# Kernel tuning notes

Hardware: AMD Instinct MI355X
Metric: run time of the kernel (lower is better)

## Reference

```python
import jax, jax.numpy as jnp
import numpy as np

BS, D, NC, N, C, K = 8192, 1024, 64, 100000, 1000, 50


def setup_inputs() -> dict:
    key = jax.random.key(0)
    k1, k2, k3, k4, k5 = jax.random.split(key, 5)
    return {
        "train_embedding": jax.random.normal(k1, (BS, D), dtype=jnp.float32),
        # concept initialized uniform in [-0.5, 0.5] as in init_concept
        "concept": jax.random.uniform(k2, (D, NC), dtype=jnp.float32, minval=-0.5, maxval=0.5),
        "bank": jax.random.normal(k3, (N, D), dtype=jnp.float32),
        "W_h": jax.random.normal(k4, (D, C), dtype=jnp.float32) * 0.02,
        "b_h": jax.random.normal(k5, (C,), dtype=jnp.float32) * 0.02,
        "topk": K,
    }


def reference(train_embedding, concept, bank, W_h, b_h, topk):
    # h_x: linear classifier head
    def h_x(z):
        return z @ W_h + b_h

    # projection onto concept subspace: C (C^T C)^{-1} C^T
    G = concept.T @ concept                      # [nc, nc]
    proj_matrix = concept @ jnp.linalg.inv(G) @ concept.T  # [D, D]
    proj = train_embedding @ proj_matrix.T       # (proj_matrix @ X^T)^T -> [bs, D]
    y_pred = h_x(proj)                           # [bs, C]
    orig_pred = h_x(train_embedding)             # [bs, C]

    # batched per-concept Euclidean distance to the whole bank: [nc, N]
    bank_sq = jnp.sum(bank * bank, axis=1)       # [N]
    con_sq = jnp.sum(concept * concept, axis=0)  # [nc]
    d2 = con_sq[:, None] - 2.0 * (concept.T @ bank.T) + bank_sq[None, :]
    dist = jnp.sqrt(jnp.maximum(d2, 0.0))
    # topk SMALLEST distances per concept
    _, idx = jax.lax.top_k(-dist, topk)          # idx: [nc, k]
    knn = bank[idx]                              # [nc, k, D] gather

    # L_sparse_1: mean over concepts of (c . mean_k knn)
    dots = jnp.einsum('dn,nkd->n', concept, knn) / topk  # [nc]
    L_sparse_1 = jnp.mean(dots)

    nc = concept.shape[1]
    eye = jnp.eye(nc, dtype=concept.dtype)
    L_sparse_2 = jnp.mean(G * (1.0 - eye))       # off-diagonal mean
    norm_metrics = jnp.mean(G * eye)             # diagonal mean

    return (orig_pred, y_pred, L_sparse_1, L_sparse_2, norm_metrics)
```

## Files before the change

### kernel.cpp

```cpp
#include <hip/hip_runtime.h>
#include <cstddef>

#define BSZ   8192
#define DIM   1024
#define NCON  64
#define NBANK 100000
#define NCLS  1000
#define TOPK  50
#define NCHUNK 32
#define CHUNK  3125
#define CHUNKP 3328

#define Y_OFF 8192000
#define S_OFF 16384000

typedef __attribute__((ext_vector_type(8))) short bf16x8;
typedef __attribute__((ext_vector_type(4))) float f32x4;

__device__ __forceinline__ short f2bf(float x) {
    unsigned u = __builtin_bit_cast(unsigned, x);
    unsigned r = (u + 0x7fffu + ((u >> 16) & 1u)) >> 16;
    return (short)r;
}

__device__ __forceinline__ bf16x8 pack8(f32x4 a, f32x4 b) {
    bf16x8 p;
    p[0] = f2bf(a[0]); p[1] = f2bf(a[1]); p[2] = f2bf(a[2]); p[3] = f2bf(a[3]);
    p[4] = f2bf(b[0]); p[5] = f2bf(b[1]); p[6] = f2bf(b[2]); p[7] = f2bf(b[3]);
    return p;
}

__device__ __forceinline__ void gload16(const void* g, void* l) {
    __builtin_amdgcn_global_load_lds(
        (__attribute__((address_space(1))) void*)g,
        (__attribute__((address_space(3))) void*)l,
        16, 0, 0);
}

__global__ void __launch_bounds__(256) prep_kernel(const float* __restrict__ cpt,
                                                   const float* __restrict__ Wh,
                                                   short* __restrict__ WhT,
                                                   short* __restrict__ cptT) {
    __shared__ short Ts[64][65];
    int b = blockIdx.x;
    int t = threadIdx.x;
    if (b < 256) {
        int k0 = (b & 15) * 64, n0 = (b >> 4) * 64;
        #pragma unroll
        for (int i = 0; i < 16; ++i) {
            int u = i * 256 + t;
            int kL = u >> 6, nL = u & 63;
            int n = n0 + nL;
            Ts[kL][nL] = (n < NCLS) ? f2bf(Wh[(size_t)(k0 + kL) * NCLS + n]) : (short)0;
        }
        __syncthreads();
        #pragma unroll
        for (int i = 0; i < 16; ++i) {
            int u = i * 256 + t;
            int nL = u >> 6, kL = u & 63;
            WhT[(size_t)(n0 + nL) * DIM + k0 + kL] = Ts[kL][nL];
        }
    } else {
        int q = b - 256;
        #pragma unroll
        for (int i = 0; i < 16; ++i) {
            int u = q * 4096 + i * 256 + t;
            int d = u >> 6, n = u & 63;
            cptT[n * DIM + d] = f2bf(cpt[u]);
        }
    }
}

__global__ void __launch_bounds__(256) mid_kernel(const float* __restrict__ bank,
                                                  const float* __restrict__ X,
                                                  const short* __restrict__ cptT,
                                                  const short* __restrict__ WhT,
                                                  short* __restrict__ Xbf,
                                                  short* __restrict__ XCbf,
                                                  float* __restrict__ key,
                                                  float* __restrict__ bank_sq,
                                                  short* __restrict__ MbfT,
                                                  float* __restrict__ G,
                                                  short* __restrict__ invGbf) {
    __shared__ __align__(16) char smem[40960];
    int b = blockIdx.x;
    int t = threadIdx.x;
    int wid = t >> 6, l = t & 63, lr = l & 15, lg = l >> 4;
    if (b < 8) {
        int c0 = b * 128;
        f32x4 acc[4][2] = {};
        for (int kk = 0; kk < DIM; kk += 32) {
            bf16x8 af[4], bfr[2];
            #pragma unroll
            for (int mi = 0; mi < 4; ++mi)
                af[mi] = *(const bf16x8*)(cptT + (mi * 16 + lr) * DIM + kk + lg * 8);
            #pragma unroll
            for (int ni = 0; ni < 2; ++ni)
                bfr[ni] = *(const bf16x8*)(WhT + (size_t)(c0 + wid * 32 + ni * 16 + lr) * DIM + kk + lg * 8);
            #pragma unroll
            for (int mi = 0; mi < 4; ++mi)
                #pragma unroll
                for (int ni = 0; ni < 2; ++ni)
                    acc[mi][ni] = __builtin_amdgcn_mfma_f32_16x16x32_bf16(af[mi], bfr[ni], acc[mi][ni], 0, 0, 0);
        }
        #pragma unroll
        for (int mi = 0; mi < 4; ++mi)
            #pragma unroll
            for (int ni = 0; ni < 2; ++ni)
                #pragma unroll
                for (int r = 0; r < 4; ++r) {
                    int m = mi * 16 + lg * 4 + r;
                    int c = c0 + wid * 32 + ni * 16 + lr;
                    MbfT[(size_t)c * NCON + m] = f2bf(acc[mi][ni][r]);
                }
    } else if (b == 8) {
        float* rowk = (float*)smem;
        float* fk = (float*)(smem + 256);
        f32x4 acc[4] = {};
        for (int kk = 0; kk < DIM; kk += 32) {
            bf16x8 af[4], bfr;
            #pragma unroll
            for (int mi = 0; mi < 4; ++mi)
                af[mi] = *(const bf16x8*)(cptT + (mi * 16 + lr) * DIM + kk + lg * 8);
            bfr = *(const bf16x8*)(cptT + (wid * 16 + lr) * DIM + kk + lg * 8);
            #pragma unroll
            for (int mi = 0; mi < 4; ++mi)
                acc[mi] = __builtin_amdgcn_mfma_f32_16x16x32_bf16(af[mi], bfr, acc[mi], 0, 0, 0);
        }
        #pragma unroll
        for (int mi = 0; mi < 4; ++mi)
            #pragma unroll
            for (int r = 0; r < 4; ++r)
                G[(mi * 16 + lg * 4 + r) * 64 + wid * 16 + lr] = acc[mi][r];
        __syncthreads();
        float myA[16];
        #pragma unroll
        for (int s = 0; s < 16; ++s) myA[s] = G[(4 * s + wid) * 64 + l];
        #pragma unroll
        for (int k = 0; k < 64; ++k) {
            if (wid == (k & 3)) rowk[l] = myA[k >> 2];
            if (l == k) {
                #pragma unroll
                for (int s = 0; s < 16; ++s) fk[4 * s + wid] = myA[s];
            }
            __syncthreads();
            float ip = 1.f / rowk[k];
            float rv = rowk[l];
            #pragma unroll
            for (int s = 0; s < 16; ++s) {
                int i = 4 * s + wid;
                float fv = fk[i];
                float nv;
                if (i == k && l == k)      nv = ip;
                else if (i == k)           nv = rv * ip;
                else if (l == k)           nv = -fv * ip;
                else                       nv = myA[s] - fv * (rv * ip);
                myA[s] = nv;
            }
            __syncthreads();
        }
        #pragma unroll
        for (int s = 0; s < 16; ++s) invGbf[(4 * s + wid) * 64 + l] = f2bf(myA[s]);
    } else if (b < 73) {
        int r0 = (b - 9) * 128;
        int r_[2];
        const float* xrow[2];
        #pragma unroll
        for (int ni = 0; ni < 2; ++ni) {
            r_[ni] = r0 + wid * 32 + ni * 16 + lr;
            xrow[ni] = X + (size_t)r_[ni] * DIM + lg * 8;
        }
        f32x4 acc[4][2] = {};
        for (int kk = 0; kk < DIM; kk += 32) {
            bf16x8 af[4];
            #pragma unroll
            for (int mi = 0; mi < 4; ++mi)
                af[mi] = *(const bf16x8*)(cptT + (mi * 16 + lr) * DIM + kk + lg * 8);
            #pragma unroll
            for (int ni = 0; ni < 2; ++ni) {
                f32x4 a = *(const f32x4*)(xrow[ni] + kk);
                f32x4 c = *(const f32x4*)(xrow[ni] + kk + 4);
                bf16x8 pk = pack8(a, c);
                *(bf16x8*)(Xbf + (size_t)r_[ni] * DIM + kk + lg * 8) = pk;
                #pragma unroll
                for (int mi = 0; mi < 4; ++mi)
                    acc[mi][ni] = __builtin_amdgcn_mfma_f32_16x16x32_bf16(af[mi], pk, acc[mi][ni], 0, 0, 0);
            }
        }
        #pragma unroll
        for (int mi = 0; mi < 4; ++mi)
            #pragma unroll
            for (int ni = 0; ni < 2; ++ni)
                #pragma unroll
                for (int r = 0; r < 4; ++r) {
                    int m = mi * 16 + lg * 4 + r;
                    XCbf[(size_t)r_[ni] * NCON + m] = f2bf(acc[mi][ni][r]);
                }
    } else {
        int j0 = (b - 73) * 128;
        int bj[4], bs[4];
        #pragma unroll
        for (int i = 0; i < 4; ++i) {
            int flat = i * 4096 + wid * 1024 + l * 16;
            bj[i] = flat >> 7;
            bs[i] = ((flat >> 4) & 7) ^ (bj[i] & 7);
        }
        int cflat = wid * 1024 + l * 16;
        int cm = cflat >> 6;
        int cs = ((cflat >> 4) & 3) ^ (cm & 3);
        f32x4 acc[4][2] = {};
        float sq[2] = {0.f, 0.f};
        int jrow[2];
        #pragma unroll
        for (int ni = 0; ni < 2; ++ni) jrow[ni] = wid * 32 + ni * 16 + lr;
        #pragma unroll
        for (int i = 0; i < 4; ++i) {
            int jr = j0 + bj[i]; if (jr >= NBANK) jr = NBANK - 1;
            gload16(bank + (size_t)jr * DIM + bs[i] * 4, smem + i * 4096 + wid * 1024);
        }
        gload16(cptT + cm * DIM + cs * 8, smem + 32768 + wid * 1024);
        int buf = 0;
        for (int kk = 0; kk < DIM; kk += 32) {
            __syncthreads();
            int kn = kk + 32;
            int nb = buf ^ 1;
            if (kn < DIM) {
                #pragma unroll
                for (int i = 0; i < 4; ++i) {
                    int jr = j0 + bj[i]; if (jr >= NBANK) jr = NBANK - 1;
                    gload16(bank + (size_t)jr * DIM + kn + bs[i] * 4,
                            smem + nb * 16384 + i * 4096 + wid * 1024);
                }
                gload16(cptT + cm * DIM + kn + cs * 8, smem + 32768 + nb * 4096 + wid * 1024);
            }
            const float* bT = (const float*)(smem + buf * 16384);
            const short* cS = (const short*)(smem + 32768 + buf * 4096);
            bf16x8 af[4];
            #pragma unroll
            for (int mi = 0; mi < 4; ++mi) {
                int m = mi * 16 + lr;
                af[mi] = *(const bf16x8*)(cS + m * 32 + ((lg ^ (m & 3)) << 3));
            }
            #pragma unroll
            for (int ni = 0; ni < 2; ++ni) {
                int j = jrow[ni];
                int g0 = lg * 2, g1 = lg * 2 + 1;
                f32x4 a = *(const f32x4*)(bT + j * 32 + ((g0 ^ (j & 7)) << 2));
                f32x4 c = *(const f32x4*)(bT + j * 32 + ((g1 ^ (j & 7)) << 2));
                sq[ni] += a[0]*a[0] + a[1]*a[1] + a[2]*a[2] + a[3]*a[3]
                        + c[0]*c[0] + c[1]*c[1] + c[2]*c[2] + c[3]*c[3];
                bf16x8 pk = pack8(a, c);
                #pragma unroll
                for (int mi = 0; mi < 4; ++mi)
                    acc[mi][ni] = __builtin_amdgcn_mfma_f32_16x16x32_bf16(af[mi], pk, acc[mi][ni], 0, 0, 0);
            }
            buf ^= 1;
        }
        #pragma unroll
        for (int ni = 0; ni < 2; ++ni) {
            float s = sq[ni];
            s += __shfl_xor(s, 16);
            s += __shfl_xor(s, 32);
            sq[ni] = s;
            int j = j0 + jrow[ni];
            if (j < NBANK && lg == 0) bank_sq[j] = s;
        }
        #pragma unroll
        for (int mi = 0; mi < 4; ++mi)
            #pragma unroll
            for (int ni = 0; ni < 2; ++ni) {
                int j = j0 + jrow[ni];
                if (j < NBANK) {
                    #pragma unroll
                    for (int r = 0; r < 4; ++r) {
                        int m = mi * 16 + lg * 4 + r;
                        key[(size_t)m * NBANK + j] = sq[ni] - 2.f * acc[mi][ni][r];
                    }
                }
            }
    }
}

__global__ void __launch_bounds__(256) topA_kernel(const float* __restrict__ key,
                                                   float* __restrict__ cand_v,
                                                   int* __restrict__ cand_j,
                                                   const short* __restrict__ invGbf,
                                                   const short* __restrict__ MbfT,
                                                   short* __restrict__ M2T) {
    __shared__ float vals[CHUNKP];
    __shared__ float wv[4];
    __shared__ int wj[4];
    int b = blockIdx.x;
    int t = threadIdx.x;
    if (b < 2048) {
        int n = b >> 5;
        int c = b & 31;
        int base = c * CHUNK;
        const float* row = key + (size_t)n * NBANK + base;
        float lv = __builtin_inff();
        int lj = 0x7fffffff;
        #pragma unroll 13
        for (int i = 0; i < 13; ++i) {
            int j = t + i * 256;
            float v = (j < CHUNK) ? row[j] : __builtin_inff();
            vals[j] = v;
            if (v < lv) { lv = v; lj = j; }
        }
        __syncthreads();
        float* cv = cand_v + (size_t)b * TOPK;
        int* cj = cand_j + (size_t)b * TOPK;
        for (int it = 0; it < TOPK; ++it) {
            float bv = lv; int bj = lj;
            #pragma unroll
            for (int o = 32; o > 0; o >>= 1) {
                float ov = __shfl_down(bv, o);
                int oj = __shfl_down(bj, o);
                if (ov < bv || (ov == bv && oj < bj)) { bv = ov; bj = oj; }
            }
            if ((t & 63) == 0) { wv[t >> 6] = bv; wj[t >> 6] = bj; }
            __syncthreads();
            float gv = wv[0]; int gj = wj[0];
            #pragma unroll
            for (int w2 = 1; w2 < 4; ++w2)
                if (wv[w2] < gv || (wv[w2] == gv && wj[w2] < gj)) { gv = wv[w2]; gj = wj[w2]; }
            if (t == 0) { cv[it] = gv; cj[it] = base + gj; }
            if (t == (gj & 255)) {
                vals[gj] = __builtin_inff();
                lv = __builtin_inff(); lj = 0x7fffffff;
                #pragma unroll 13
                for (int i = 0; i < 13; ++i) {
                    int j = t + i * 256;
                    float v = vals[j];
                    if (v < lv) { lv = v; lj = j; }
                }
            }
            __syncthreads();
        }
    } else {
        int c0 = (b - 2048) * 128;
        int wid = t >> 6, l = t & 63, lr = l & 15, lg = l >> 4;
        f32x4 acc[4][2] = {};
        #pragma unroll
        for (int ks = 0; ks < 2; ++ks) {
            bf16x8 af[4], bfr[2];
            #pragma unroll
            for (int mi = 0; mi < 4; ++mi)
                af[mi] = *(const bf16x8*)(invGbf + (mi * 16 + lr) * NCON + ks * 32 + lg * 8);
            #pragma unroll
            for (int ni = 0; ni < 2; ++ni)
                bfr[ni] = *(const bf16x8*)(MbfT + (size_t)(c0 + wid * 32 + ni * 16 + lr) * NCON + ks * 32 + lg * 8);
            #pragma unroll
            for (int mi = 0; mi < 4; ++mi)
                #pragma unroll
                for (int ni = 0; ni < 2; ++ni)
                    acc[mi][ni] = __builtin_amdgcn_mfma_f32_16x16x32_bf16(af[mi], bfr[ni], acc[mi][ni], 0, 0, 0);
        }
        #pragma unroll
        for (int mi = 0; mi < 4; ++mi)
            #pragma unroll
            for (int ni = 0; ni < 2; ++ni)
                #pragma unroll
                for (int r = 0; r < 4; ++r) {
                    int n = mi * 16 + lg * 4 + r;
                    int c = c0 + wid * 32 + ni * 16 + lr;
                    M2T[(size_t)c * NCON + n] = f2bf(acc[mi][ni][r]);
                }
    }
}

__global__ void __launch_bounds__(256) pred_kernel(const short* __restrict__ Xbf,
                                                   const short* __restrict__ WhT,
                                                   const short* __restrict__ XCbf,
                                                   const short* __restrict__ M2T,
                                                   const float* __restrict__ bh,
                                                   const float* __restrict__ cand_v,
                                                   const int* __restrict__ cand_j,
                                                   const float* __restrict__ bank_sq,
                                                   float* __restrict__ orig,
                                                   float* __restrict__ ypred,
                                                   float* __restrict__ dots) {
    __shared__ __align__(16) char smem[32768];
    int b = blockIdx.x;
    int t = threadIdx.x;
    int wid = t >> 6, l = t & 63, lr = l & 15, lg = l >> 4;
    if (b < 512) {
        short* As = (short*)smem;
        short* Bs = (short*)(smem + 16384);
        int c0 = (b & 7) * 128;
        int r0 = (b >> 3) * 128;
        int wr = wid >> 1, wc = wid & 1;
        int srow_off = l >> 3;
        int scol = ((l & 7) ^ (l >> 3)) * 8;
        f32x4 acc[4][4] = {};
        for (int kk = 0; kk < DIM; kk += 64) {
            if (kk) __syncthreads();
            #pragma unroll
            for (int i = 0; i < 4; ++i) {
                int si = wid * 4 + i;
                int row = si * 8 + srow_off;
                gload16(Xbf + (size_t)(r0 + row) * DIM + kk + scol, As + si * 512);
                gload16(WhT + (size_t)(c0 + row) * DIM + kk + scol, Bs + si * 512);
            }
            __syncthreads();
            #pragma unroll
            for (int ks = 0; ks < 2; ++ks) {
                bf16x8 af[4], bfr[4];
                #pragma unroll
                for (int mi = 0; mi < 4; ++mi) {
                    int rr = wr * 64 + mi * 16 + lr;
                    int slot = (ks * 4 + lg) ^ (rr & 7);
                    af[mi] = *(const bf16x8*)(As + rr * 64 + slot * 8);
                }
                #pragma unroll
                for (int ni = 0; ni < 4; ++ni) {
                    int cc = wc * 64 + ni * 16 + lr;
                    int slot = (ks * 4 + lg) ^ (cc & 7);
                    bfr[ni] = *(const bf16x8*)(Bs + cc * 64 + slot * 8);
                }
                #pragma unroll
                for (int mi = 0; mi < 4; ++mi)
                    #pragma unroll
                    for (int ni = 0; ni < 4; ++ni)
                        acc[mi][ni] = __builtin_amdgcn_mfma_f32_16x16x32_bf16(af[mi], bfr[ni], acc[mi][ni], 0, 0, 0);
            }
        }
        #pragma unroll
        for (int mi = 0; mi < 4; ++mi)
            #pragma unroll
            for (int ni = 0; ni < 4; ++ni) {
                int col = c0 + wc * 64 + ni * 16 + lr;
                if (col < NCLS) {
                    float bias = bh[col];
                    #pragma unroll
                    for (int r = 0; r < 4; ++r) {
                        int row = r0 + wr * 64 + mi * 16 + lg * 4 + r;
                        orig[(size_t)row * NCLS + col] = acc[mi][ni][r] + bias;
                    }
                }
            }
    } else if (b < 1024) {
        int q = b - 512;
        int c0 = (q & 7) * 128;
        int r0 = (q >> 3) * 128;
        int wr = wid >> 1, wc = wid & 1;
        f32x4 acc[4][4] = {};
        #pragma unroll
        for (int ks = 0; ks < 2; ++ks) {
            bf16x8 af[4], bfr[4];
            #pragma unroll
            for (int mi = 0; mi < 4; ++mi)
                af[mi] = *(const bf16x8*)(XCbf + (size_t)(r0 + wr * 64 + mi * 16 + lr) * NCON + ks * 32 + lg * 8);
            #pragma unroll
            for (int ni = 0; ni < 4; ++ni)
                bfr[ni] = *(const bf16x8*)(M2T + (size_t)(c0 + wc * 64 + ni * 16 + lr) * NCON + ks * 32 + lg * 8);
            #pragma unroll
            for (int mi = 0; mi < 4; ++mi)
                #pragma unroll
                for (int ni = 0; ni < 4; ++ni)
                    acc[mi][ni] = __builtin_amdgcn_mfma_f32_16x16x32_bf16(af[mi], bfr[ni], acc[mi][ni], 0, 0, 0);
        }
        #pragma unroll
        for (int mi = 0; mi < 4; ++mi)
            #pragma unroll
            for (int ni = 0; ni < 4; ++ni) {
                int col = c0 + wc * 64 + ni * 16 + lr;
                if (col < NCLS) {
                    float bias = bh[col];
                    #pragma unroll
                    for (int r = 0; r < 4; ++r) {
                        int row = r0 + wr * 64 + mi * 16 + lg * 4 + r;
                        ypred[(size_t)row * NCLS + col] = acc[mi][ni][r] + bias;
                    }
                }
            }
    } else {
        int n = b - 1024;
        const int NC2 = NCHUNK * TOPK;
        float* vals = (float*)smem;
        int* gidx = (int*)(smem + 6400);
        float* wv = (float*)(smem + 12800);
        int* wj = (int*)(smem + 12816);
        int* wl = (int*)(smem + 12832);
        for (int j = t; j < NC2; j += 256) {
            vals[j] = cand_v[(size_t)n * NC2 + j];
            gidx[j] = cand_j[(size_t)n * NC2 + j];
        }
        __syncthreads();
        float sum = 0.f;
        for (int it = 0; it < TOPK; ++it) {
            float bv = __builtin_inff();
            int bj = 0x7fffffff;
            int bl = -1;
            #pragma unroll 7
            for (int j = t; j < NC2; j += 256) {
                float v = vals[j];
                int gj = gidx[j];
                if (v < bv || (v == bv && gj < bj)) { bv = v; bj = gj; bl = j; }
            }
            #pragma unroll
            for (int o = 32; o > 0; o >>= 1) {
                float ov = __shfl_down(bv, o);
                int oj = __shfl_down(bj, o);
                int ol = __shfl_down(bl, o);
                if (ov < bv || (ov == bv && oj < bj)) { bv = ov; bj = oj; bl = ol; }
            }
            if ((t & 63) == 0) { wv[t >> 6] = bv; wj[t >> 6] = bj; wl[t >> 6] = bl; }
            __syncthreads();
            if (t == 0) {
                #pragma unroll
                for (int w2 = 1; w2 < 4; ++w2)
                    if (wv[w2] < bv || (wv[w2] == bv && wj[w2] < bj)) { bv = wv[w2]; bj = wj[w2]; bl = wl[w2]; }
                sum += 0.5f * (bank_sq[bj] - bv);
                vals[bl] = __builtin_inff();
            }
            __syncthreads();
        }
        if (t == 0) dots[n] = sum / (float)TOPK;
    }
}

__global__ void __launch_bounds__(256) fin_kernel(const float* __restrict__ G,
                                                  const float* __restrict__ dots,
                                                  float* __restrict__ out3) {
    __shared__ float r1[256], r2[256], r3[256];
    int t = threadIdx.x;
    float sd = 0.f, so = 0.f;
    for (int u = t; u < 4096; u += 256) {
        float g = G[u];
        if ((u >> 6) == (u & 63)) sd += g; else so += g;
    }
    float s1 = (t < NCON) ? dots[t] : 0.f;
    r1[t] = sd; r2[t] = so; r3[t] = s1;
    __syncthreads();
    for (int o = 128; o > 0; o >>= 1) {
        if (t < o) { r1[t] += r1[t + o]; r2[t] += r2[t + o]; r3[t] += r3[t + o]; }
        __syncthreads();
    }
    if (t == 0) {
        out3[0] = r3[0] / 64.f;
        out3[1] = r2[0] / 4096.f;
        out3[2] = r1[0] / 4096.f;
    }
}

extern "C" void kernel_launch(void* const* d_in, const int* in_sizes, int n_in,
                              void* d_out, int out_size, void* d_ws, size_t ws_size,
                              hipStream_t stream) {
    const float* X    = (const float*)d_in[0];
    const float* cpt  = (const float*)d_in[1];
    const float* bank = (const float*)d_in[2];
    const float* Wh   = (const float*)d_in[3];
    const float* bh   = (const float*)d_in[4];
    float* out = (float*)d_out;

    float* orig  = out;
    float* ypred = out + Y_OFF;
    float* out3  = out + S_OFF;

    char* w = (char*)d_ws;
    short* Xbf    = (short*)(w);
    short* WhT    = (short*)(w + 16777216);
    short* cptT   = (short*)(w + 18874368);
    short* XCbf   = (short*)(w + 19005440);
    short* M2T    = (short*)(w + 20054016);
    float* key    = (float*)(w + 20185088);
    float* bank_sq= (float*)(w + 45785088);
    float* G      = (float*)(w + 46185472);
    short* invGbf = (short*)(w + 46201856);
    short* MbfT   = (short*)(w + 46210048);
    float* cand_v = (float*)(w + 46341120);
    int*   cand_j = (int*)  (w + 46750720);
    float* dots   = (float*)(w + 47160320);

    prep_kernel<<<272, 256, 0, stream>>>(cpt, Wh, WhT, cptT);
    mid_kernel<<<73 + 782, 256, 0, stream>>>(bank, X, cptT, WhT, Xbf, XCbf, key, bank_sq, MbfT, G, invGbf);
    topA_kernel<<<2056, 256, 0, stream>>>(key, cand_v, cand_j, invGbf, MbfT, M2T);
    pred_kernel<<<1088, 256, 0, stream>>>(Xbf, WhT, XCbf, M2T, bh, cand_v, cand_j, bank_sq, orig, ypred, dots);
    fin_kernel<<<1, 256, 0, stream>>>(G, dots, out3);
}
```

Before: 404.2 us.

## Retile bank distance GEMM to 64 rows per block with 64-wide K steps

The bank-distance branch of mid_kernel now gives each block 64 bank rows instead of 128, which doubles the block count to 1563 so more CUs stay busy. The K step goes from 32 to 64, halving the number of barriers and pipeline stages, with a matching 16-way XOR swizzle and a larger concept tile in shared memory. Each wave holds one 16-row fragment instead of two. The trade-off is that the concept tile is reloaded by twice as many blocks, and shared memory per block grows to 48KB, which may lower occupancy.

New measurement: 378.9 us (median of 2 runs). 1.07x faster.

```diff
diff --git a/kernel.cpp b/kernel.cpp
--- a/kernel.cpp
+++ b/kernel.cpp
@@ -10,6 +10,7 @@
 #define NCHUNK 32
 #define CHUNK  3125
 #define CHUNKP 3328
+#define NDIST 1563
 
 #define Y_OFF 8192000
 #define S_OFF 16384000
@@ -82,7 +83,7 @@
                                                   short* __restrict__ MbfT,
                                                   float* __restrict__ G,
                                                   short* __restrict__ invGbf) {
-    __shared__ __align__(16) char smem[40960];
+    __shared__ __align__(16) char smem[49152];
     int b = blockIdx.x;
     int t = threadIdx.x;
     int wid = t >> 6, l = t & 63, lr = l & 15, lg = l >> 4;
@@ -197,87 +198,84 @@
                     XCbf[(size_t)r_[ni] * NCON + m] = f2bf(acc[mi][ni][r]);
                 }
     } else {
-        int j0 = (b - 73) * 128;
-        int bj[4], bs[4];
+        int j0 = (b - 73) * 64;
+        int bj4[4], bs4[4];
         #pragma unroll
         for (int i = 0; i < 4; ++i) {
             int flat = i * 4096 + wid * 1024 + l * 16;
-            bj[i] = flat >> 7;
-            bs[i] = ((flat >> 4) & 7) ^ (bj[i] & 7);
-        }
-        int cflat = wid * 1024 + l * 16;
-        int cm = cflat >> 6;
-        int cs = ((cflat >> 4) & 3) ^ (cm & 3);
-        f32x4 acc[4][2] = {};
-        float sq[2] = {0.f, 0.f};
-        int jrow[2];
-        #pragma unroll
-        for (int ni = 0; ni < 2; ++ni) jrow[ni] = wid * 32 + ni * 16 + lr;
+            bj4[i] = flat >> 8;
+            bs4[i] = ((flat >> 4) & 15) ^ (bj4[i] & 15);
+        }
+        int cm2[2], cs2[2];
+        #pragma unroll
+        for (int i = 0; i < 2; ++i) {
+            int flat = i * 4096 + wid * 1024 + l * 16;
+            cm2[i] = flat >> 7;
+            cs2[i] = ((flat >> 4) & 7) ^ (cm2[i] & 7);
+        }
+        int jl = wid * 16 + lr;
+        f32x4 acc[4] = {};
+        float sq = 0.f;
         #pragma unroll
         for (int i = 0; i < 4; ++i) {
-            int jr = j0 + bj[i]; if (jr >= NBANK) jr = NBANK - 1;
-            gload16(bank + (size_t)jr * DIM + bs[i] * 4, smem + i * 4096 + wid * 1024);
-        }
-        gload16(cptT + cm * DIM + cs * 8, smem + 32768 + wid * 1024);
+            int jr = j0 + bj4[i]; if (jr >= NBANK) jr = NBANK - 1;
+            gload16(bank + (size_t)jr * DIM + bs4[i] * 4, smem + i * 4096 + wid * 1024);
+        }
+        #pragma unroll
+        for (int i = 0; i < 2; ++i)
+            gload16(cptT + cm2[i] * DIM + cs2[i] * 8, smem + 32768 + i * 4096 + wid * 1024);
         int buf = 0;
-        for (int kk = 0; kk < DIM; kk += 32) {
-            __syncthreads();
-            int kn = kk + 32;
+        for (int kk = 0; kk < DIM; kk += 64) {
+            __syncthreads();
+            int kn = kk + 64;
             int nb = buf ^ 1;
             if (kn < DIM) {
                 #pragma unroll
                 for (int i = 0; i < 4; ++i) {
-                    int jr = j0 + bj[i]; if (jr >= NBANK) jr = NBANK - 1;
-                    gload16(bank + (size_t)jr * DIM + kn + bs[i] * 4,
+                    int jr = j0 + bj4[i]; if (jr >= NBANK) jr = NBANK - 1;
+                    gload16(bank + (size_t)jr * DIM + kn + bs4[i] * 4,
                             smem + nb * 16384 + i * 4096 + wid * 1024);
                 }
-                gload16(cptT + cm * DIM + kn + cs * 8, smem + 32768 + nb * 4096 + wid * 1024);
+                #pragma unroll
+                for (int i = 0; i < 2; ++i)
+                    gload16(cptT + cm2[i] * DIM + kn + cs2[i] * 8,
+                            smem + 32768 + nb * 8192 + i * 4096 + wid * 1024);
             }
             const float* bT = (const float*)(smem + buf * 16384);
-            const short* cS = (const short*)(smem + 32768 + buf * 4096);
-            bf16x8 af[4];
-            #pragma unroll
-            for (int mi = 0; mi < 4; ++mi) {
-                int m = mi * 16 + lr;
-                af[mi] = *(const bf16x8*)(cS + m * 32 + ((lg ^ (m & 3)) << 3));
-            }
-            #pragma unroll
-            for (int ni = 0; ni < 2; ++ni) {
-                int j = jrow[ni];
-                int g0 = lg * 2, g1 = lg * 2 + 1;
-                f32x4 a = *(const f32x4*)(bT + j * 32 + ((g0 ^ (j & 7)) << 2));
-                f32x4 c = *(const f32x4*)(bT + j * 32 + ((g1 ^ (j & 7)) << 2));
-                sq[ni] += a[0]*a[0] + a[1]*a[1] + a[2]*a[2] + a[3]*a[3]
-                        + c[0]*c[0] + c[1]*c[1] + c[2]*c[2] + c[3]*c[3];
+            const short* cS = (const short*)(smem + 32768 + buf * 8192);
+            #pragma unroll
+            for (int ks = 0; ks < 2; ++ks) {
+                bf16x8 af[4];
+                #pragma unroll
+                for (int mi = 0; mi < 4; ++mi) {
+                    int m = mi * 16 + lr;
+                    af[mi] = *(const bf16x8*)(cS + m * 64 + (((ks * 4 + lg) ^ (m & 7)) << 3));
+                }
+                int g0 = ks * 8 + lg * 2;
+                f32x4 a = *(const f32x4*)(bT + jl * 64 + ((g0 ^ (jl & 15)) << 2));
+                f32x4 c = *(const f32x4*)(bT + jl * 64 + (((g0 + 1) ^ (jl & 15)) << 2));
+                sq += a[0]*a[0] + a[1]*a[1] + a[2]*a[2] + a[3]*a[3]
+                    + c[0]*c[0] + c[1]*c[1] + c[2]*c[2] + c[3]*c[3];
                 bf16x8 pk = pack8(a, c);
                 #pragma unroll
                 for (int mi = 0; mi < 4; ++mi)
-                    acc[mi][ni] = __builtin_amdgcn_mfma_f32_16x16x32_bf16(af[mi], pk, acc[mi][ni], 0, 0, 0);
+                    acc[mi] = __builtin_amdgcn_mfma_f32_16x16x32_bf16(af[mi], pk, acc[mi], 0, 0, 0);
             }
             buf ^= 1;
         }
-        #pragma unroll
-        for (int ni = 0; ni < 2; ++ni) {
-            float s = sq[ni];
-            s += __shfl_xor(s, 16);
-            s += __shfl_xor(s, 32);
-            sq[ni] = s;
-            int j = j0 + jrow[ni];
-            if (j < NBANK && lg == 0) bank_sq[j] = s;
-        }
-        #pragma unroll
-        for (int mi = 0; mi < 4; ++mi)
-            #pragma unroll
-            for (int ni = 0; ni < 2; ++ni) {
-                int j = j0 + jrow[ni];
-                if (j < NBANK) {
-                    #pragma unroll
-                    for (int r = 0; r < 4; ++r) {
-                        int m = mi * 16 + lg * 4 + r;
-                        key[(size_t)m * NBANK + j] = sq[ni] - 2.f * acc[mi][ni][r];
-                    }
-                }
-            }
+        sq += __shfl_xor(sq, 16);
+        sq += __shfl_xor(sq, 32);
+        int j = j0 + jl;
+        if (j < NBANK) {
+            if (lg == 0) bank_sq[j] = sq;
+            #pragma unroll
+            for (int mi = 0; mi < 4; ++mi)
+                #pragma unroll
+                for (int r = 0; r < 4; ++r) {
+                    int m = mi * 16 + lg * 4 + r;
+                    key[(size_t)m * NBANK + j] = sq - 2.f * acc[mi][r];
+                }
+        }
     }
 }
 
@@ -573,7 +571,7 @@
     float* dots   = (float*)(w + 47160320);
 
     prep_kernel<<<272, 256, 0, stream>>>(cpt, Wh, WhT, cptT);
-    mid_kernel<<<73 + 782, 256, 0, stream>>>(bank, X, cptT, WhT, Xbf, XCbf, key, bank_sq, MbfT, G, invGbf);
+    mid_kernel<<<73 + NDIST, 256, 0, stream>>>(bank, X, cptT, WhT, Xbf, XCbf, key, bank_sq, MbfT, G, invGbf);
     topA_kernel<<<2056, 256, 0, stream>>>(key, cand_v, cand_j, invGbf, MbfT, M2T);
     pred_kernel<<<1088, 256, 0, stream>>>(Xbf, WhT, XCbf, M2T, bh, cand_v, cand_j, bank_sq, orig, ypred, dots);
     fin_kernel<<<1, 256, 0, stream>>>(G, dots, out3);
```
